# Kernel optimization log

Hardware: AMD Instinct MI355X
Metric: run time of the kernel (lower is better)

## Reference

```python
import jax, jax.numpy as jnp
import numpy as np

N, E, IN_DIM, HID = 100000, 1600000, 128, 64


def setup_inputs() -> dict:
    key = jax.random.key(0)
    ks = jax.random.split(key, 10)
    inv = lambda f: 1.0 / np.sqrt(f)
    return {
        "x": jax.random.normal(ks[0], (N, IN_DIM), jnp.float32),
        "edge_index": jax.random.randint(ks[1], (2, E), 0, N, dtype=jnp.int32),
        "fc_w": jax.random.normal(ks[2], (IN_DIM, HID), jnp.float32) * inv(IN_DIM),
        "fc_b": jnp.zeros((HID,), jnp.float32),
        "conv1_w": jax.random.normal(ks[3], (HID, HID), jnp.float32) * inv(HID),
        "conv1_b": jnp.zeros((HID,), jnp.float32),
        "conv2_w": jax.random.normal(ks[4], (HID, HID), jnp.float32) * inv(HID),
        "conv2_b": jnp.zeros((HID,), jnp.float32),
        "node_w": jax.random.normal(ks[5], (HID, 1), jnp.float32) * inv(HID),
        "node_b": jnp.zeros((1,), jnp.float32),
        "edge_w": jax.random.normal(ks[6], (2 * HID, 1), jnp.float32) * inv(2 * HID),
        "edge_b": jnp.zeros((1,), jnp.float32),
    }


def _gcn_norm(row, col):
    # PyG GCNConv default: add self-loops, symmetric D^-1/2 (A+I) D^-1/2 norm.
    loops = jnp.arange(N, dtype=row.dtype)
    rows = jnp.concatenate([row, loops])
    cols = jnp.concatenate([col, loops])
    deg = jax.ops.segment_sum(jnp.ones(rows.shape[0], jnp.float32), cols, num_segments=N)
    dinv = jax.lax.rsqrt(jnp.maximum(deg, 1.0))  # deg >= 1 due to self-loops
    norm = dinv[rows] * dinv[cols]  # [E+N]
    return rows, cols, norm


def _gcn_conv(h, rows, cols, norm, W, b):
    m = h @ W                                   # [N, HID] transform first (out==in dim)
    agg = jax.ops.segment_sum(m[rows] * norm[:, None], cols, num_segments=N)
    return agg + b


def reference(x, edge_index, fc_w, fc_b, conv1_w, conv1_b, conv2_w, conv2_b,
              node_w, node_b, edge_w, edge_b):
    # Dropout layers act as identity in eval mode.
    row, col = edge_index[0], edge_index[1]
    rows, cols, norm = _gcn_norm(row, col)

    h = x @ fc_w + fc_b                          # [N, HID]
    h = jax.nn.relu(_gcn_conv(h, rows, cols, norm, conv1_w, conv1_b))
    h = jax.nn.relu(_gcn_conv(h, rows, cols, norm, conv2_w, conv2_b))

    node_score = jax.nn.sigmoid(h @ node_w + node_b)  # [N, 1]

    # edge_score = sigmoid(cat([h[row], h[col]]) @ edge_w + b)
    # == sigmoid(h[row] @ edge_w[:HID] + h[col] @ edge_w[HID:] + b)
    s_src = h @ edge_w[:HID]                     # [N, 1]
    s_dst = h @ edge_w[HID:]                     # [N, 1]
    edge_score = jax.nn.sigmoid(s_src[row] + s_dst[col] + edge_b)  # [E, 1]
    return edge_score, node_score
```

## Files before the change

### kernel.cpp

```cpp
#include <hip/hip_runtime.h>
#include <math.h>

constexpr int NN  = 100000;
constexpr int EE  = 1600000;
constexpr int IND = 128;
constexpr int HID = 64;

constexpr int NBUCK = (NN + 127) / 128;
constexpr int CAP   = 3840;
constexpr int CHUNK = 4096;
constexpr int NTILE = NN / 16;
constexpr int NCB   = (EE + CHUNK - 1) / CHUNK;
constexpr int ZOFF  = NN << 7;

using bf16x8 = __attribute__((ext_vector_type(8))) short;
using f32x4v = __attribute__((ext_vector_type(4))) float;

__device__ __forceinline__ unsigned short f2bf(float f) {
    union { float f; unsigned int u; } v; v.f = f;
    unsigned int r = (v.u + 0x7FFFu + ((v.u >> 16) & 1u)) >> 16;
    return (unsigned short)r;
}
__device__ __forceinline__ void unp(unsigned int u, float& lo, float& hi) {
    union { unsigned int x; float f; } a, c;
    a.x = u << 16; c.x = u & 0xFFFF0000u;
    lo = a.f; hi = c.f;
}

#define ACC4(u) do { float l_, h_; \
    unp((u).x, l_, h_); a0 += l_; a1 += h_; \
    unp((u).y, l_, h_); a2 += l_; a3 += h_; } while (0)


__global__ __launch_bounds__(256) void k_init(int* __restrict__ gcur, int* __restrict__ zrow) {
    int i = blockIdx.x * 256 + threadIdx.x;
    if (i < NBUCK) gcur[i] = 0;
    if (i < 32) zrow[i] = 0;
}


__global__ __launch_bounds__(1024) void k_bscatter(const int* __restrict__ row, const int* __restrict__ col,
                                                   int* __restrict__ gcur, int* __restrict__ ebuf,
                                                   const float* __restrict__ wfc, const float* __restrict__ bfc,
                                                   const float* __restrict__ w1, const float* __restrict__ w2,
                                                   unsigned short* __restrict__ wct, float* __restrict__ bvec,
                                                   unsigned short* __restrict__ w2t) {
    __shared__ int lhist[NBUCK];
    __shared__ int lbase[NBUCK];
    __shared__ int lcur[NBUCK];
    __shared__ int lcol[CHUNK];
    const int tx = threadIdx.x;

    if (blockIdx.x >= NCB) {
        int b = blockIdx.x - NCB;
        if (b < 8) {
            int idx = b * 1024 + tx;
            int k = idx >> 6, c = idx & 63;
            float acc = 0.f;
            #pragma unroll 8
            for (int j = 0; j < 64; ++j) acc += wfc[k * HID + j] * w1[j * HID + c];
            wct[c * IND + k] = f2bf(acc);
        } else if (b < 12) {
            int idx = (b - 8) * 1024 + tx;
            int k = idx >> 6, c = idx & 63;
            w2t[c * HID + k] = f2bf(w2[k * HID + c]);
        } else if (tx < 64) {
            float acc = 0.f;
            #pragma unroll 8
            for (int j = 0; j < 64; ++j) acc += bfc[j] * w1[j * HID + tx];
            bvec[tx] = acc;
        }
        return;
    }

    const int cbase = blockIdx.x * CHUNK;

    for (int b = tx; b < NBUCK; b += 1024) lhist[b] = 0;
    __syncthreads();

    #pragma unroll
    for (int i = 0; i < CHUNK / 1024; ++i) {
        int e = cbase + tx + i * 1024;
        int c = (e < EE) ? col[e] : -1;
        lcol[tx + i * 1024] = c;
        if (c >= 0) atomicAdd(&lhist[c >> 7], 1);
    }
    __syncthreads();

    for (int b = tx; b < NBUCK; b += 1024) {
        int c = lhist[b];
        if (c) lbase[b] = atomicAdd(&gcur[b], c);
        lcur[b] = 0;
    }
    __syncthreads();

    #pragma unroll
    for (int i = 0; i < CHUNK / 1024; ++i) {
        int e = cbase + tx + i * 1024;
        if (e < EE) {
            int c = lcol[tx + i * 1024];
            int b = c >> 7;
            int rank = atomicAdd(&lcur[b], 1);
            ebuf[b * CAP + lbase[b] + rank] = (row[e] << 7) | (c & 127);
        }
    }
}


__global__ __launch_bounds__(512) void k_bsortip(const int* __restrict__ gcur, int* __restrict__ ebuf,
                                                 int* __restrict__ bc, float* __restrict__ dinv) {
    __shared__ int ebl[CAP];
    __shared__ int h[128];
    __shared__ int sc[128];
    __shared__ int cur[128];
    const int tx = threadIdx.x;
    const int b = blockIdx.x;
    const int cnt = gcur[b];
    int* eb = ebuf + b * CAP;

    if (tx < 128) h[tx] = 0;
    for (int e = tx; e < cnt; e += 512) ebl[e] = eb[e];
    __syncthreads();
    for (int e = tx; e < cnt; e += 512) atomicAdd(&h[ebl[e] & 127], 1);
    __syncthreads();

    int np = 0;
    if (tx < 128) {
        int g = b * 128 + tx;
        int n1 = (g < NN) ? h[tx] + 1 : 0;
        np = (n1 + 15) & ~15;
        sc[tx] = np;
    }
    __syncthreads();
    #pragma unroll
    for (int o = 1; o < 128; o <<= 1) {
        int add = (tx < 128 && tx >= o) ? sc[tx - o] : 0;
        __syncthreads();
        if (tx < 128) sc[tx] += add;
        __syncthreads();
    }
    if (tx < 128) {
        int g = b * 128 + tx;
        int ex = sc[tx] - np;
        cur[tx] = ex + 1;
        if (g < NN) {
            int n1 = h[tx] + 1;
            bc[g]   = (ex << 16) | np;
            dinv[g] = rsqrtf((float)n1);
            if (ex < CAP) eb[ex] = g << 7;
            int end = ex + np; if (end > CAP) end = CAP;
            for (int p = ex + n1; p < end; ++p) eb[p] = ZOFF;
        }
    }
    __syncthreads();

    for (int e = tx; e < cnt; e += 512) {
        int v = ebl[e];
        int r = atomicAdd(&cur[v & 127], 1);
        if (r < CAP) eb[r] = v & 0xFFFFFF80;
    }
}


__global__ __launch_bounds__(256) void k_mmx(const float* __restrict__ x,
        const unsigned short* __restrict__ wct, const float* __restrict__ bvec,
        const float* __restrict__ dinv, unsigned short* __restrict__ mdb) {
    const int tx = threadIdx.x;
    const int lane = tx & 63;
    const int wv = tx >> 6;
    const int l15 = lane & 15, g = lane >> 4;
    const int tile = blockIdx.x * 4 + wv;
    if (tile >= NTILE) return;
    const int row0 = tile * 16;

    bf16x8 bf[4][4];
    #pragma unroll
    for (int t = 0; t < 4; ++t) {
        const unsigned short* bp = wct + (t * 16 + l15) * IND + g * 8;
        #pragma unroll
        for (int kc = 0; kc < 4; ++kc)
            bf[t][kc] = *(const bf16x8*)(bp + kc * 32);
    }

    const float* ap = x + (row0 + l15) * IND + g * 8;
    bf16x8 af[4];
    #pragma unroll
    for (int kc = 0; kc < 4; ++kc) {
        float4 lo = *(const float4*)(ap + kc * 32);
        float4 hi = *(const float4*)(ap + kc * 32 + 4);
        bf16x8 f;
        f[0] = (short)f2bf(lo.x); f[1] = (short)f2bf(lo.y);
        f[2] = (short)f2bf(lo.z); f[3] = (short)f2bf(lo.w);
        f[4] = (short)f2bf(hi.x); f[5] = (short)f2bf(hi.y);
        f[6] = (short)f2bf(hi.z); f[7] = (short)f2bf(hi.w);
        af[kc] = f;
    }

    f32x4v acc[4];
    #pragma unroll
    for (int t = 0; t < 4; ++t) {
        float bv = bvec[t * 16 + l15];
        acc[t][0] = bv; acc[t][1] = bv; acc[t][2] = bv; acc[t][3] = bv;
    }
    #pragma unroll
    for (int kc = 0; kc < 4; ++kc) {
        #pragma unroll
        for (int t = 0; t < 4; ++t)
            acc[t] = __builtin_amdgcn_mfma_f32_16x16x32_bf16(af[kc], bf[t][kc], acc[t], 0, 0, 0);
    }

    #pragma unroll
    for (int r = 0; r < 4; ++r) {
        int rowg = row0 + g * 4 + r;
        float di = dinv[rowg];
        #pragma unroll
        for (int t = 0; t < 4; ++t)
            mdb[rowg * HID + t * 16 + l15] = f2bf(acc[t][r] * di);
    }
}


__global__ __launch_bounds__(256) void k_mm2x(const unsigned short* __restrict__ h1b,
        const unsigned short* __restrict__ w2t, const float* __restrict__ dinv,
        unsigned short* __restrict__ mdb) {
    const int tx = threadIdx.x;
    const int lane = tx & 63;
    const int wv = tx >> 6;
    const int l15 = lane & 15, g = lane >> 4;
    const int tile = blockIdx.x * 4 + wv;
    if (tile >= NTILE) return;
    const int row0 = tile * 16;

    bf16x8 bf[4][2];
    #pragma unroll
    for (int t = 0; t < 4; ++t) {
        const unsigned short* bp = w2t + (t * 16 + l15) * HID + g * 8;
        #pragma unroll
        for (int kc = 0; kc < 2; ++kc)
            bf[t][kc] = *(const bf16x8*)(bp + kc * 32);
    }

    const unsigned short* ap = h1b + (row0 + l15) * HID + g * 8;
    bf16x8 af[2];
    af[0] = *(const bf16x8*)(ap);
    af[1] = *(const bf16x8*)(ap + 32);

    f32x4v acc[4] = {};
    #pragma unroll
    for (int kc = 0; kc < 2; ++kc) {
        #pragma unroll
        for (int t = 0; t < 4; ++t)
            acc[t] = __builtin_amdgcn_mfma_f32_16x16x32_bf16(af[kc], bf[t][kc], acc[t], 0, 0, 0);
    }

    #pragma unroll
    for (int r = 0; r < 4; ++r) {
        int rowg = row0 + g * 4 + r;
        float di = dinv[rowg];
        #pragma unroll
        for (int t = 0; t < 4; ++t)
            mdb[rowg * HID + t * 16 + l15] = f2bf(acc[t][r] * di);
    }
}


__global__ __launch_bounds__(256) void k_gather(const unsigned short* __restrict__ mdb,
                                                const int* __restrict__ ebuf, const int* __restrict__ bc,
                                                const float* __restrict__ dinv, const float* __restrict__ b,
                                                unsigned short* __restrict__ hout) {
    int lane = threadIdx.x & 63;
    int q    = lane >> 4;
    int f4   = lane & 15;
    int wid  = (blockIdx.x * blockDim.x + threadIdx.x) >> 6;
    int nwv  = (gridDim.x * blockDim.x) >> 6;
    float4 bj = *(const float4*)&b[f4 * 4];
    const char* mbase = (const char*)mdb + f4 * 8;

    for (int i = wid; i < NN; i += nwv) {
        int vv = bc[i];
        const int* prq = ebuf + (i >> 7) * CAP + (vv >> 16) + q;
        int n = vv & 0xFFFF;
        float a0 = 0.f, a1 = 0.f, a2 = 0.f, a3 = 0.f;
        for (int e = 0; e < n; e += 16) {
            int r0 = prq[e];
            int r1 = prq[e + 4];
            int r2 = prq[e + 8];
            int r3 = prq[e + 12];
            uint2 u0 = *(const uint2*)(mbase + r0);
            uint2 u1 = *(const uint2*)(mbase + r1);
            uint2 u2 = *(const uint2*)(mbase + r2);
            uint2 u3 = *(const uint2*)(mbase + r3);
            ACC4(u0); ACC4(u1); ACC4(u2); ACC4(u3);
        }
        a0 += __shfl_xor(a0, 32, 64); a1 += __shfl_xor(a1, 32, 64);
        a2 += __shfl_xor(a2, 32, 64); a3 += __shfl_xor(a3, 32, 64);
        a0 += __shfl_xor(a0, 16, 64); a1 += __shfl_xor(a1, 16, 64);
        a2 += __shfl_xor(a2, 16, 64); a3 += __shfl_xor(a3, 16, 64);

        if (q == 0) {
            float di = dinv[i];
            ushort4 o;
            o.x = f2bf(fmaxf(di * a0 + bj.x, 0.f));
            o.y = f2bf(fmaxf(di * a1 + bj.y, 0.f));
            o.z = f2bf(fmaxf(di * a2 + bj.z, 0.f));
            o.w = f2bf(fmaxf(di * a3 + bj.w, 0.f));
            *(ushort4*)&hout[i * HID + f4 * 4] = o;
        }
    }
}


__global__ __launch_bounds__(256) void k_gather2s(const unsigned short* __restrict__ mdb,
        const int* __restrict__ ebuf, const int* __restrict__ bc, const float* __restrict__ dinv,
        const float* __restrict__ b, const float* __restrict__ nw, const float* __restrict__ nb,
        const float* __restrict__ ew, float* __restrict__ out_node,
        float* __restrict__ ssrc, float* __restrict__ sdst) {
    int lane = threadIdx.x & 63;
    int q    = lane >> 4;
    int f4   = lane & 15;
    int wid  = (blockIdx.x * blockDim.x + threadIdx.x) >> 6;
    int nwv  = (gridDim.x * blockDim.x) >> 6;
    float4 bj  = *(const float4*)&b[f4 * 4];
    float4 wn  = *(const float4*)&nw[f4 * 4];
    float4 we1 = *(const float4*)&ew[f4 * 4];
    float4 we2 = *(const float4*)&ew[64 + f4 * 4];
    float nb0 = nb[0];
    const char* mbase = (const char*)mdb + f4 * 8;

    for (int i = wid; i < NN; i += nwv) {
        int vv = bc[i];
        const int* prq = ebuf + (i >> 7) * CAP + (vv >> 16) + q;
        int n = vv & 0xFFFF;
        float a0 = 0.f, a1 = 0.f, a2 = 0.f, a3 = 0.f;
        for (int e = 0; e < n; e += 16) {
            int r0 = prq[e];
            int r1 = prq[e + 4];
            int r2 = prq[e + 8];
            int r3 = prq[e + 12];
            uint2 u0 = *(const uint2*)(mbase + r0);
            uint2 u1 = *(const uint2*)(mbase + r1);
            uint2 u2 = *(const uint2*)(mbase + r2);
            uint2 u3 = *(const uint2*)(mbase + r3);
            ACC4(u0); ACC4(u1); ACC4(u2); ACC4(u3);
        }
        a0 += __shfl_xor(a0, 32, 64); a1 += __shfl_xor(a1, 32, 64);
        a2 += __shfl_xor(a2, 32, 64); a3 += __shfl_xor(a3, 32, 64);
        a0 += __shfl_xor(a0, 16, 64); a1 += __shfl_xor(a1, 16, 64);
        a2 += __shfl_xor(a2, 16, 64); a3 += __shfl_xor(a3, 16, 64);

        float di = dinv[i];
        float v0 = fmaxf(di * a0 + bj.x, 0.f);
        float v1 = fmaxf(di * a1 + bj.y, 0.f);
        float v2 = fmaxf(di * a2 + bj.z, 0.f);
        float v3 = fmaxf(di * a3 + bj.w, 0.f);

        float a  = v0 * wn.x  + v1 * wn.y  + v2 * wn.z  + v3 * wn.w;
        float s1 = v0 * we1.x + v1 * we1.y + v2 * we1.z + v3 * we1.w;
        float s2 = v0 * we2.x + v1 * we2.y + v2 * we2.z + v3 * we2.w;
        #pragma unroll
        for (int off = 8; off; off >>= 1) {
            a  += __shfl_xor(a,  off, 64);
            s1 += __shfl_xor(s1, off, 64);
            s2 += __shfl_xor(s2, off, 64);
        }
        if (lane == 0) {
            out_node[i] = 1.f / (1.f + expf(-(a + nb0)));
            ssrc[i] = s1;
            sdst[i] = s2;
        }
    }
}


__global__ __launch_bounds__(256) void k_edge(const int4* __restrict__ row4, const int4* __restrict__ col4,
                                              const float* __restrict__ ssrc, const float* __restrict__ sdst,
                                              const float* __restrict__ eb, float4* __restrict__ out4) {
    constexpr int NQ = EE / 4;
    int i = blockIdx.x * 256 + threadIdx.x;
    if (i >= NQ) return;
    float eb0 = eb[0];
    int4 r = row4[i], c = col4[i];
    float4 o;
    float z;
    z = ssrc[r.x] + sdst[c.x] + eb0; o.x = 1.f / (1.f + expf(-z));
    z = ssrc[r.y] + sdst[c.y] + eb0; o.y = 1.f / (1.f + expf(-z));
    z = ssrc[r.z] + sdst[c.z] + eb0; o.z = 1.f / (1.f + expf(-z));
    z = ssrc[r.w] + sdst[c.w] + eb0; o.w = 1.f / (1.f + expf(-z));
    out4[i] = o;
}

extern "C" void kernel_launch(void* const* d_in, const int* in_sizes, int n_in,
                              void* d_out, int out_size, void* d_ws, size_t ws_size,
                              hipStream_t stream) {
    const float* x    = (const float*)d_in[0];
    const int*   ei   = (const int*)d_in[1];
    const float* fc_w = (const float*)d_in[2];
    const float* fc_b = (const float*)d_in[3];
    const float* c1w  = (const float*)d_in[4];
    const float* c1b  = (const float*)d_in[5];
    const float* c2w  = (const float*)d_in[6];
    const float* c2b  = (const float*)d_in[7];
    const float* nw   = (const float*)d_in[8];
    const float* nb   = (const float*)d_in[9];
    const float* ew   = (const float*)d_in[10];
    const float* eb   = (const float*)d_in[11];
    const int* row = ei;
    const int* col = ei + EE;

    constexpr int NP = 100352;
    float* ws   = (float*)d_ws;
    float* dinv = ws;
    int*   bc   = (int*)(ws + NP);
    int*   gcur = (int*)(ws + 2 * NP);
    unsigned short* wct = (unsigned short*)(ws + 2 * NP + 1024);
    float* bvec = ws + 2 * NP + 1024 + 4096;
    unsigned short* w2t = (unsigned short*)(bvec + 128);
    int*   ebuf = (int*)(bvec + 128 + 2048);
    float* Areg = (float*)(ebuf + NBUCK * CAP);
    unsigned short* h1b = (unsigned short*)Areg;
    unsigned short* Bbf = (unsigned short*)(Areg + (size_t)NN * HID / 2);
    int* zrow = (int*)((char*)Bbf + (size_t)NN * HID * 2);
    float* ssrc = Areg;
    float* sdst = Areg + NP;

    float* out_edge = (float*)d_out;
    float* out_node = out_edge + EE;

    const int nbQ = (EE / 4 + 255) / 256;
    const int nbM = (NTILE + 3) / 4;

    k_init    <<<(NBUCK + 255) / 256, 256, 0, stream>>>(gcur, zrow);
    k_bscatter<<<NCB + 13, 1024, 0, stream>>>(row, col, gcur, ebuf,
                                              fc_w, fc_b, c1w, c2w, wct, bvec, w2t);
    k_bsortip <<<NBUCK, 512, 0, stream>>>(gcur, ebuf, bc, dinv);

    k_mmx   <<<nbM, 256, 0, stream>>>(x, wct, bvec, dinv, Bbf);
    k_gather<<<2048, 256, 0, stream>>>(Bbf, ebuf, bc, dinv, c1b, h1b);

    k_mm2x    <<<nbM, 256, 0, stream>>>(h1b, w2t, dinv, Bbf);
    k_gather2s<<<2048, 256, 0, stream>>>(Bbf, ebuf, bc, dinv, c2b,
                                         nw, nb, ew, out_node, ssrc, sdst);

    k_edge<<<nbQ, 256, 0, stream>>>((const int4*)row, (const int4*)col,
                                    ssrc, sdst, eb, (float4*)out_edge);
}
```

Measured before the change: 172.4 us.

## Fuse first GCN aggregation with second layer matmul via shared-memory tile

Merges the layer-1 neighbor gather and the layer-2 dense transform into one kernel. Each block aggregates 64 nodes into a swizzled LDS tile, then runs MFMA on it and writes the scaled bf16 messages directly. This removes the h1 round trip through global memory and one kernel launch. In exchange it gives up the persistent grid-stride gather in favour of one block per 64 nodes, which may load-balance worse, and it needs a second buffer and zero row.

```diff
diff --git a/kernel.cpp b/kernel.cpp
--- a/kernel.cpp
+++ b/kernel.cpp
@@ -32,10 +32,11 @@
     unp((u).y, l_, h_); a2 += l_; a3 += h_; } while (0)
 
 
-__global__ __launch_bounds__(256) void k_init(int* __restrict__ gcur, int* __restrict__ zrow) {
+__global__ __launch_bounds__(256) void k_init(int* __restrict__ gcur, int* __restrict__ zrow1,
+                                              int* __restrict__ zrow2) {
     int i = blockIdx.x * 256 + threadIdx.x;
     if (i < NBUCK) gcur[i] = 0;
-    if (i < 32) zrow[i] = 0;
+    if (i < 32) { zrow1[i] = 0; zrow2[i] = 0; }
 }
 
 
@@ -220,92 +221,86 @@
 }
 
 
-__global__ __launch_bounds__(256) void k_mm2x(const unsigned short* __restrict__ h1b,
-        const unsigned short* __restrict__ w2t, const float* __restrict__ dinv,
-        unsigned short* __restrict__ mdb) {
+__global__ __launch_bounds__(256) void k_gmm(const unsigned short* __restrict__ mdb,
+        const int* __restrict__ ebuf, const int* __restrict__ bc, const float* __restrict__ dinv,
+        const float* __restrict__ b1, const unsigned short* __restrict__ w2t,
+        unsigned short* __restrict__ md2) {
+    __shared__ unsigned short sh[64 * 64];
     const int tx = threadIdx.x;
     const int lane = tx & 63;
     const int wv = tx >> 6;
+    const int q = lane >> 4, f4 = lane & 15;
+    const int nbase = blockIdx.x * 64;
+    float4 bj = *(const float4*)&b1[f4 * 4];
+    const char* mbase = (const char*)mdb + f4 * 8;
+
+    #pragma unroll 1
+    for (int t = 0; t < 16; ++t) {
+        int i = nbase + wv * 16 + t;
+        if (i < NN) {
+            int vv = bc[i];
+            const int* prq = ebuf + (i >> 7) * CAP + (vv >> 16) + q;
+            int n = vv & 0xFFFF;
+            float a0 = 0.f, a1 = 0.f, a2 = 0.f, a3 = 0.f;
+            for (int e = 0; e < n; e += 16) {
+                int r0 = prq[e];
+                int r1 = prq[e + 4];
+                int r2 = prq[e + 8];
+                int r3 = prq[e + 12];
+                uint2 u0 = *(const uint2*)(mbase + r0);
+                uint2 u1 = *(const uint2*)(mbase + r1);
+                uint2 u2 = *(const uint2*)(mbase + r2);
+                uint2 u3 = *(const uint2*)(mbase + r3);
+                ACC4(u0); ACC4(u1); ACC4(u2); ACC4(u3);
+            }
+            a0 += __shfl_xor(a0, 32, 64); a1 += __shfl_xor(a1, 32, 64);
+            a2 += __shfl_xor(a2, 32, 64); a3 += __shfl_xor(a3, 32, 64);
+            a0 += __shfl_xor(a0, 16, 64); a1 += __shfl_xor(a1, 16, 64);
+            a2 += __shfl_xor(a2, 16, 64); a3 += __shfl_xor(a3, 16, 64);
+
+            if (q == 0) {
+                int il = wv * 16 + t;
+                float di = dinv[i];
+                ushort4 o;
+                o.x = f2bf(fmaxf(di * a0 + bj.x, 0.f));
+                o.y = f2bf(fmaxf(di * a1 + bj.y, 0.f));
+                o.z = f2bf(fmaxf(di * a2 + bj.z, 0.f));
+                o.w = f2bf(fmaxf(di * a3 + bj.w, 0.f));
+                *(ushort4*)((char*)sh + il * 128 + ((f4 * 8) ^ ((il & 7) << 4))) = o;
+            }
+        }
+    }
+    __syncthreads();
+
+    const int row0g = nbase + wv * 16;
+    if (row0g >= NN) return;
     const int l15 = lane & 15, g = lane >> 4;
-    const int tile = blockIdx.x * 4 + wv;
-    if (tile >= NTILE) return;
-    const int row0 = tile * 16;
-
-    bf16x8 bf[4][2];
+
+    bf16x8 bfr[4][2];
     #pragma unroll
     for (int t = 0; t < 4; ++t) {
         const unsigned short* bp = w2t + (t * 16 + l15) * HID + g * 8;
-        #pragma unroll
-        for (int kc = 0; kc < 2; ++kc)
-            bf[t][kc] = *(const bf16x8*)(bp + kc * 32);
-    }
-
-    const unsigned short* ap = h1b + (row0 + l15) * HID + g * 8;
-    bf16x8 af[2];
-    af[0] = *(const bf16x8*)(ap);
-    af[1] = *(const bf16x8*)(ap + 32);
+        bfr[t][0] = *(const bf16x8*)(bp);
+        bfr[t][1] = *(const bf16x8*)(bp + 32);
+    }
+    const int arow = wv * 16 + l15;
+    const char* shb = (const char*)sh + arow * 128;
+    bf16x8 af0 = *(const bf16x8*)(shb + ((g * 16)      ^ ((arow & 7) << 4)));
+    bf16x8 af1 = *(const bf16x8*)(shb + ((g * 16 + 64) ^ ((arow & 7) << 4)));
 
     f32x4v acc[4] = {};
     #pragma unroll
-    for (int kc = 0; kc < 2; ++kc) {
-        #pragma unroll
-        for (int t = 0; t < 4; ++t)
-            acc[t] = __builtin_amdgcn_mfma_f32_16x16x32_bf16(af[kc], bf[t][kc], acc[t], 0, 0, 0);
-    }
-
+    for (int t = 0; t < 4; ++t) {
+        acc[t] = __builtin_amdgcn_mfma_f32_16x16x32_bf16(af0, bfr[t][0], acc[t], 0, 0, 0);
+        acc[t] = __builtin_amdgcn_mfma_f32_16x16x32_bf16(af1, bfr[t][1], acc[t], 0, 0, 0);
+    }
     #pragma unroll
     for (int r = 0; r < 4; ++r) {
-        int rowg = row0 + g * 4 + r;
+        int rowg = row0g + g * 4 + r;
         float di = dinv[rowg];
         #pragma unroll
         for (int t = 0; t < 4; ++t)
-            mdb[rowg * HID + t * 16 + l15] = f2bf(acc[t][r] * di);
-    }
-}
-
-
-__global__ __launch_bounds__(256) void k_gather(const unsigned short* __restrict__ mdb,
-                                                const int* __restrict__ ebuf, const int* __restrict__ bc,
-                                                const float* __restrict__ dinv, const float* __restrict__ b,
-                                                unsigned short* __restrict__ hout) {
-    int lane = threadIdx.x & 63;
-    int q    = lane >> 4;
-    int f4   = lane & 15;
-    int wid  = (blockIdx.x * blockDim.x + threadIdx.x) >> 6;
-    int nwv  = (gridDim.x * blockDim.x) >> 6;
-    float4 bj = *(const float4*)&b[f4 * 4];
-    const char* mbase = (const char*)mdb + f4 * 8;
-
-    for (int i = wid; i < NN; i += nwv) {
-        int vv = bc[i];
-        const int* prq = ebuf + (i >> 7) * CAP + (vv >> 16) + q;
-        int n = vv & 0xFFFF;
-        float a0 = 0.f, a1 = 0.f, a2 = 0.f, a3 = 0.f;
-        for (int e = 0; e < n; e += 16) {
-            int r0 = prq[e];
-            int r1 = prq[e + 4];
-            int r2 = prq[e + 8];
-            int r3 = prq[e + 12];
-            uint2 u0 = *(const uint2*)(mbase + r0);
-            uint2 u1 = *(const uint2*)(mbase + r1);
-            uint2 u2 = *(const uint2*)(mbase + r2);
-            uint2 u3 = *(const uint2*)(mbase + r3);
-            ACC4(u0); ACC4(u1); ACC4(u2); ACC4(u3);
-        }
-        a0 += __shfl_xor(a0, 32, 64); a1 += __shfl_xor(a1, 32, 64);
-        a2 += __shfl_xor(a2, 32, 64); a3 += __shfl_xor(a3, 32, 64);
-        a0 += __shfl_xor(a0, 16, 64); a1 += __shfl_xor(a1, 16, 64);
-        a2 += __shfl_xor(a2, 16, 64); a3 += __shfl_xor(a3, 16, 64);
-
-        if (q == 0) {
-            float di = dinv[i];
-            ushort4 o;
-            o.x = f2bf(fmaxf(di * a0 + bj.x, 0.f));
-            o.y = f2bf(fmaxf(di * a1 + bj.y, 0.f));
-            o.z = f2bf(fmaxf(di * a2 + bj.z, 0.f));
-            o.w = f2bf(fmaxf(di * a3 + bj.w, 0.f));
-            *(ushort4*)&hout[i * HID + f4 * 4] = o;
-        }
+            md2[rowg * HID + t * 16 + l15] = f2bf(acc[t][r] * di);
     }
 }
 
@@ -407,7 +402,8 @@
     const int* row = ei;
     const int* col = ei + EE;
 
-    constexpr int NP = 100352;
+    constexpr int NP    = 100352;
+    constexpr int MDSZ  = NN * HID / 2 + 32;
     float* ws   = (float*)d_ws;
     float* dinv = ws;
     int*   bc   = (int*)(ws + NP);
@@ -416,29 +412,31 @@
     float* bvec = ws + 2 * NP + 1024 + 4096;
     unsigned short* w2t = (unsigned short*)(bvec + 128);
     int*   ebuf = (int*)(bvec + 128 + 2048);
-    float* Areg = (float*)(ebuf + NBUCK * CAP);
-    unsigned short* h1b = (unsigned short*)Areg;
-    unsigned short* Bbf = (unsigned short*)(Areg + (size_t)NN * HID / 2);
-    int* zrow = (int*)((char*)Bbf + (size_t)NN * HID * 2);
-    float* ssrc = Areg;
-    float* sdst = Areg + NP;
+    float* md1f = (float*)(ebuf + NBUCK * CAP);
+    float* md2f = md1f + MDSZ;
+    unsigned short* md1 = (unsigned short*)md1f;
+    unsigned short* md2 = (unsigned short*)md2f;
+    int* zrow1 = (int*)((char*)md1 + (size_t)NN * HID * 2);
+    int* zrow2 = (int*)((char*)md2 + (size_t)NN * HID * 2);
+    float* ssrc = md1f;
+    float* sdst = md1f + NP;
 
     float* out_edge = (float*)d_out;
     float* out_node = out_edge + EE;
 
     const int nbQ = (EE / 4 + 255) / 256;
     const int nbM = (NTILE + 3) / 4;
-
-    k_init    <<<(NBUCK + 255) / 256, 256, 0, stream>>>(gcur, zrow);
+    const int nbF = (NN + 63) / 64;
+
+    k_init    <<<(NBUCK + 255) / 256, 256, 0, stream>>>(gcur, zrow1, zrow2);
     k_bscatter<<<NCB + 13, 1024, 0, stream>>>(row, col, gcur, ebuf,
                                               fc_w, fc_b, c1w, c2w, wct, bvec, w2t);
     k_bsortip <<<NBUCK, 512, 0, stream>>>(gcur, ebuf, bc, dinv);
 
-    k_mmx   <<<nbM, 256, 0, stream>>>(x, wct, bvec, dinv, Bbf);
-    k_gather<<<2048, 256, 0, stream>>>(Bbf, ebuf, bc, dinv, c1b, h1b);
-
-    k_mm2x    <<<nbM, 256, 0, stream>>>(h1b, w2t, dinv, Bbf);
-    k_gather2s<<<2048, 256, 0, stream>>>(Bbf, ebuf, bc, dinv, c2b,
+    k_mmx<<<nbM, 256, 0, stream>>>(x, wct, bvec, dinv, md1);
+    k_gmm<<<nbF, 256, 0, stream>>>(md1, ebuf, bc, dinv, c1b, w2t, md2);
+
+    k_gather2s<<<2048, 256, 0, stream>>>(md2, ebuf, bc, dinv, c2b,
                                          nw, nb, ew, out_node, ssrc, sdst);
 
     k_edge<<<nbQ, 256, 0, stream>>>((const int4*)row, (const int4*)col,
```

New measurement: 168.5 us, median of 2. -2.3%, faster.
